# Optimization experiments

Hardware: AMD Instinct MI355X
Metric: run time of the kernel (lower is better)

Reference implementation:

```python
import jax, jax.numpy as jnp
import numpy as np
import math

B, S, D = 16, 4096, 64

def setup_inputs() -> dict:
    key = jax.random.key(0)
    kq, kk, kv = jax.random.split(key, 3)
    query = jax.random.normal(kq, (B, S, D), dtype=jnp.float32)
    k_ = jax.random.normal(kk, (B, S, D), dtype=jnp.float32)
    value = jax.random.normal(kv, (B, S, D), dtype=jnp.float32)
    # causal mask: 1 = allowed, 0 = masked (set to -inf), broadcast over batch
    mask = jnp.tril(jnp.ones((S, S), dtype=jnp.int32))[None, :, :]
    return {"query": query, "key": k_, "value": value, "mask": mask, "key_dim": D}

def reference(query, key, value, mask, key_dim):
    # scores: [B, S, S] = Q @ K^T / sqrt(dk)
    scores = jnp.einsum('bqd,bkd->bqk', query, key) / math.sqrt(key_dim)
    scores = jnp.where(mask == 0, -jnp.inf, scores)
    attn = jax.nn.softmax(scores, axis=-1)
    return jnp.einsum('bqk,bkd->bqd', attn, value)
```

## Files before the change

### kernel.cpp

```cpp
#include <hip/hip_runtime.h>

typedef _Float16 half8 __attribute__((ext_vector_type(8)));
typedef float f32x4 __attribute__((ext_vector_type(4)));
typedef unsigned int uint32x2 __attribute__((ext_vector_type(2)));

union Frag { half8 v; unsigned int u32[4]; uint4 u4; };
union Pack4 { _Float16 h[4]; unsigned int u[2]; };

constexpr int S = 4096;
constexpr int D = 64;
constexpr int NB = 16;
constexpr int LTS = 72;

__device__ __forceinline__ float ex2(float x) {
#if __has_builtin(__builtin_amdgcn_exp2f)
    return __builtin_amdgcn_exp2f(x);
#else
    return exp2f(x);
#endif
}

__global__ __launch_bounds__(256)
void prep_kernel(const float* __restrict__ K, const float* __restrict__ V,
                 _Float16* __restrict__ K16, _Float16* __restrict__ VT) {
    __shared__ float tl[64 * 66];
    const int tid = threadIdx.x;
    const int s0 = blockIdx.x * 64;
    const int b  = blockIdx.y;
    const float* Kb = K + ((size_t)b * S + s0) * D;
    const float* Vb = V + ((size_t)b * S + s0) * D;
    _Float16* K16b = K16 + ((size_t)b * S + s0) * D;

    #pragma unroll
    for (int i = 0; i < 2; ++i) {
        int e8 = tid + 256 * i;
        float4 a = ((const float4*)Kb)[2 * e8];
        float4 c = ((const float4*)Kb)[2 * e8 + 1];
        Frag f;
        f.v[0]=(_Float16)a.x; f.v[1]=(_Float16)a.y; f.v[2]=(_Float16)a.z; f.v[3]=(_Float16)a.w;
        f.v[4]=(_Float16)c.x; f.v[5]=(_Float16)c.y; f.v[6]=(_Float16)c.z; f.v[7]=(_Float16)c.w;
        ((uint4*)K16b)[e8] = f.u4;
    }
    #pragma unroll
    for (int i = 0; i < 4; ++i) {
        int fi = tid + 256 * i;
        int r = fi >> 4, c4 = (fi & 15) << 2;
        float4 v = *(const float4*)(Vb + (size_t)r * D + c4);
        float2* p = (float2*)&tl[r * 66 + c4];
        p[0] = make_float2(v.x, v.y);
        p[1] = make_float2(v.z, v.w);
    }
    __syncthreads();
    _Float16* VTb = VT + (size_t)b * D * S;
    #pragma unroll
    for (int i = 0; i < 2; ++i) {
        int fi = tid + 256 * i;
        int d = fi >> 3, s8 = (fi & 7) << 3;
        Frag f;
        #pragma unroll
        for (int j = 0; j < 8; ++j) f.v[j] = (_Float16)tl[(s8 + j) * 66 + d];
        *(uint4*)(VTb + (size_t)d * S + s0 + s8) = f.u4;
    }
}

template <int SPLIT>
__device__ __forceinline__
void fattn_body(const float* __restrict__ Q, const _Float16* __restrict__ K16,
                const _Float16* __restrict__ VT16, float* __restrict__ Out,
                _Float16* __restrict__ OP, float* __restrict__ LP,
                int b, int J, int t0, int t1, int h) {
    __shared__ __align__(16) _Float16 kt[64 * LTS];
    __shared__ __align__(16) _Float16 vt[64 * LTS];

    const int tid  = threadIdx.x;
    const int lane = tid & 63;
    const int wave = tid >> 6;
    const int ln   = lane & 15;
    const int quad = lane >> 4;

    const float* Qb = Q + (size_t)b * S * D;
    const _Float16* Kb = K16 + (size_t)b * S * D;
    const _Float16* VTb = VT16 + (size_t)b * D * S;

    const float qscale = 0.125f * 1.44269504088896340736f;
    const int qrow_base = J * 128 + wave * 32;
    const int tw = (qrow_base + 31) >> 6;

    Frag qf[2][2];
    #pragma unroll
    for (int qg = 0; qg < 2; ++qg) {
        const float* qrow = Qb + (size_t)(qrow_base + qg * 16 + ln) * D + quad * 8;
        #pragma unroll
        for (int ks = 0; ks < 2; ++ks) {
            float4 a = *(const float4*)(qrow + ks * 32);
            float4 c = *(const float4*)(qrow + ks * 32 + 4);
            Frag f;
            f.v[0]=(_Float16)(a.x*qscale); f.v[1]=(_Float16)(a.y*qscale);
            f.v[2]=(_Float16)(a.z*qscale); f.v[3]=(_Float16)(a.w*qscale);
            f.v[4]=(_Float16)(c.x*qscale); f.v[5]=(_Float16)(c.y*qscale);
            f.v[6]=(_Float16)(c.z*qscale); f.v[7]=(_Float16)(c.w*qscale);
            qf[qg][ks] = f;
        }
    }

    f32x4 o[2][4] = {};
    float l_acc[2] = {0.f, 0.f};

    for (int t = t0; t < t1; ++t) {
        const int k0 = t * 64;
        __syncthreads();

        #pragma unroll
        for (int i = 0; i < 2; ++i) {
            int fi = tid + 256 * i;
            int r = fi >> 3, c8 = (fi & 7) << 3;
            uint4 kk = *(const uint4*)(Kb + (size_t)(k0 + r) * D + c8);
            uint4 vv = *(const uint4*)(VTb + (size_t)r * S + k0 + c8);
            *(uint4*)(kt + r * LTS + c8) = kk;
            *(uint4*)(vt + r * LTS + c8) = vv;
        }
        __syncthreads();

        #pragma unroll
        for (int ks = 0; ks < 2; ++ks) {
            unsigned w[2][2][2];
            #pragma unroll
            for (int cl = 0; cl < 2; ++cl) {
                const int ct = ks * 2 + cl;
                Frag kf0, kf1;
                kf0.u4 = *(const uint4*)(kt + (ct * 16 + ln) * LTS + quad * 8);
                kf1.u4 = *(const uint4*)(kt + (ct * 16 + ln) * LTS + 32 + quad * 8);
                #pragma unroll
                for (int qg = 0; qg < 2; ++qg) {
                    f32x4 acc = {0.f, 0.f, 0.f, 0.f};
                    acc = __builtin_amdgcn_mfma_f32_16x16x32_f16(kf0.v, qf[qg][0].v, acc, 0, 0, 0);
                    acc = __builtin_amdgcn_mfma_f32_16x16x32_f16(kf1.v, qf[qg][1].v, acc, 0, 0, 0);
                    if (t >= tw) {
                        int keyb = k0 + ct * 16 + quad * 4;
                        int qrow = qrow_base + qg * 16 + ln;
                        #pragma unroll
                        for (int r = 0; r < 4; ++r)
                            if (keyb + r > qrow) acc[r] = -1e30f;
                    }
                    float p0 = ex2(acc[0]), p1 = ex2(acc[1]);
                    float p2 = ex2(acc[2]), p3 = ex2(acc[3]);
                    l_acc[qg] += (p0 + p1) + (p2 + p3);
                    Pack4 pk;
                    pk.h[0] = (_Float16)p0; pk.h[1] = (_Float16)p1;
                    pk.h[2] = (_Float16)p2; pk.h[3] = (_Float16)p3;
                    w[qg][cl][0] = pk.u[0];
                    w[qg][cl][1] = pk.u[1];
                }
            }

            Frag pf[2];
            #pragma unroll
            for (int qg = 0; qg < 2; ++qg) {
                unsigned x0 = w[qg][0][0], y0 = w[qg][1][0];
                unsigned x1 = w[qg][0][1], y1 = w[qg][1][1];
#if __has_builtin(__builtin_amdgcn_permlane32_swap) && __has_builtin(__builtin_amdgcn_permlane16_swap)
                uint32x2 r;
                r = __builtin_amdgcn_permlane32_swap(x0, y0, false, false); x0 = r[0]; y0 = r[1];
                r = __builtin_amdgcn_permlane32_swap(x1, y1, false, false); x1 = r[0]; y1 = r[1];
                r = __builtin_amdgcn_permlane16_swap(x0, y0, false, false); x0 = r[0]; y0 = r[1];
                r = __builtin_amdgcn_permlane16_swap(x1, y1, false, false); x1 = r[0]; y1 = r[1];
#else
                asm volatile("s_nop 1\n\tv_permlane32_swap_b32 %0, %1\n\ts_nop 1"
                             : "+v"(x0), "+v"(y0));
                asm volatile("v_permlane32_swap_b32 %0, %1\n\ts_nop 1"
                             : "+v"(x1), "+v"(y1));
                asm volatile("v_permlane16_swap_b32 %0, %1\n\ts_nop 1"
                             : "+v"(x0), "+v"(y0));
                asm volatile("v_permlane16_swap_b32 %0, %1\n\ts_nop 1"
                             : "+v"(x1), "+v"(y1));
#endif
                pf[qg].u32[0] = x0; pf[qg].u32[1] = x1;
                pf[qg].u32[2] = y0; pf[qg].u32[3] = y1;
            }

            #pragma unroll
            for (int sub = 0; sub < 4; ++sub) {
                Frag vf;
                vf.u4 = *(const uint4*)(vt + (sub * 16 + ln) * LTS + ks * 32 + quad * 8);
                #pragma unroll
                for (int qg = 0; qg < 2; ++qg)
                    o[qg][sub] = __builtin_amdgcn_mfma_f32_16x16x32_f16(pf[qg].v, vf.v, o[qg][sub], 0, 0, 0);
            }
        }
    }

    float lf[2];
    #pragma unroll
    for (int qg = 0; qg < 2; ++qg) {
        float x = l_acc[qg];
        x += __shfl_xor(x, 16, 64);
        x += __shfl_xor(x, 32, 64);
        lf[qg] = x;
    }

    if (SPLIT) {
        _Float16* OPb = OP + (size_t)(((b * 32 + J) * 4 + h)) * 8192;
        float* LPb = LP + (size_t)(((b * 32 + J) * 4 + h)) * 128;
        #pragma unroll
        for (int qg = 0; qg < 2; ++qg) {
            if (quad == 0) LPb[wave * 32 + qg * 16 + ln] = lf[qg];
            #pragma unroll
            for (int r = 0; r < 4; ++r) {
                float lrow = __shfl(lf[qg], quad * 4 + r, 64);
                float inv = (lrow > 0.f) ? (1.0f / lrow) : 0.f;
                #pragma unroll
                for (int sub = 0; sub < 4; ++sub)
                    OPb[(wave * 32 + qg * 16 + quad * 4 + r) * 64 + sub * 16 + ln] =
                        (_Float16)(o[qg][sub][r] * inv);
            }
        }
    } else {
        float* Ob = Out + (size_t)b * S * D;
        #pragma unroll
        for (int qg = 0; qg < 2; ++qg) {
            #pragma unroll
            for (int r = 0; r < 4; ++r) {
                float lrow = __shfl(lf[qg], quad * 4 + r, 64);
                float inv = 1.0f / lrow;
                #pragma unroll
                for (int sub = 0; sub < 4; ++sub)
                    Ob[(size_t)(qrow_base + qg * 16 + quad * 4 + r) * D + sub * 16 + ln] =
                        o[qg][sub][r] * inv;
            }
        }
    }
}

__global__ __launch_bounds__(256, 4)
void fattn_split_kernel(const float* __restrict__ Q, const _Float16* __restrict__ K16,
                        const _Float16* __restrict__ VT16,
                        _Float16* __restrict__ OP, float* __restrict__ LP) {
    const int bx = blockIdx.x;
    const int J = 31 - (bx >> 6);
    const int h = (bx >> 4) & 3;
    const int b = bx & 15;
    const int n  = 2 * J + 2;
    const int t0 = (h * n) >> 2;
    const int t1 = ((h + 1) * n) >> 2;
    fattn_body<1>(Q, K16, VT16, nullptr, OP, LP, b, J, t0, t1, h);
}

__global__ __launch_bounds__(256, 4)
void fattn_kernel(const float* __restrict__ Q, const _Float16* __restrict__ K16,
                  const _Float16* __restrict__ VT16, float* __restrict__ Out) {
    const int bx = blockIdx.x;
    const int J = 31 - (bx >> 4);
    const int b = bx & 15;
    fattn_body<0>(Q, K16, VT16, Out, nullptr, nullptr, b, J, 0, 2 * J + 2, 0);
}

__global__ __launch_bounds__(256)
void reduce_kernel(const _Float16* __restrict__ OP, const float* __restrict__ LP,
                   float* __restrict__ Out) {
    const int rb = blockIdx.x;
    const int b  = rb & 15;
    const int J  = rb >> 4;
    const int tid = threadIdx.x;
    const _Float16* p = OP + (size_t)(b * 32 + J) * 4 * 8192;
    const float* l = LP + (size_t)(b * 32 + J) * 4 * 128;
    float* Ob = Out + (size_t)b * S * D + (size_t)J * 8192;
    #pragma unroll
    for (int i = 0; i < 4; ++i) {
        int e8 = tid + 256 * i;
        int q  = e8 >> 3;
        float lw[4], lsum = 0.f;
        #pragma unroll
        for (int hh = 0; hh < 4; ++hh) { lw[hh] = l[hh * 128 + q]; lsum += lw[hh]; }
        float inv = 1.0f / lsum;
        float acc[8] = {};
        #pragma unroll
        for (int hh = 0; hh < 4; ++hh) {
            half8 v = *(const half8*)(p + (size_t)hh * 8192 + e8 * 8);
            #pragma unroll
            for (int j = 0; j < 8; ++j) acc[j] += lw[hh] * (float)v[j];
        }
        float4 r0, r1;
        r0.x = acc[0]*inv; r0.y = acc[1]*inv; r0.z = acc[2]*inv; r0.w = acc[3]*inv;
        r1.x = acc[4]*inv; r1.y = acc[5]*inv; r1.z = acc[6]*inv; r1.w = acc[7]*inv;
        ((float4*)Ob)[2 * e8]     = r0;
        ((float4*)Ob)[2 * e8 + 1] = r1;
    }
}

extern "C" void kernel_launch(void* const* d_in, const int* in_sizes, int n_in,
                              void* d_out, int out_size, void* d_ws, size_t ws_size,
                              hipStream_t stream) {
    const float* Q = (const float*)d_in[0];
    const float* K = (const float*)d_in[1];
    const float* V = (const float*)d_in[2];
    float* O = (float*)d_out;

    const size_t prepBytes = (size_t)NB * S * D * 2;
    _Float16* K16  = (_Float16*)d_ws;
    _Float16* VT16 = (_Float16*)((char*)d_ws + prepBytes);

    const size_t opOff = 2 * prepBytes;
    const size_t opBytes = (size_t)NB * 32 * 4 * 8192 * 2;
    const size_t lpOff = opOff + opBytes;
    const size_t lpBytes = (size_t)NB * 32 * 4 * 128 * 4;
    const size_t need = lpOff + lpBytes;

    hipLaunchKernelGGL(prep_kernel, dim3(S / 64, NB), dim3(256), 0, stream, K, V, K16, VT16);

    if (ws_size >= need) {
        _Float16* OP = (_Float16*)((char*)d_ws + opOff);
        float* LP = (float*)((char*)d_ws + lpOff);
        hipLaunchKernelGGL(fattn_split_kernel, dim3(128 * NB), dim3(256), 0, stream,
                           Q, K16, VT16, OP, LP);
        hipLaunchKernelGGL(reduce_kernel, dim3(32 * NB), dim3(256), 0, stream, OP, LP, O);
    } else {
        hipLaunchKernelGGL(fattn_kernel, dim3(32 * NB), dim3(256), 0, stream, Q, K16, VT16, O);
    }
}
```

Before: 187.6 us.

## Prefetch next K/V tile into registers and pack probabilities with cvt_pkrtz

Global loads of the next K and V^T tile are issued into registers right after the shared-memory barrier, so their latency overlaps the current tile's MFMA and exp work. Each iteration then only stores the already-loaded registers into LDS. Separately, the fp32-to-fp16 conversion of probabilities uses packed round-toward-zero conversion, halving the conversion instructions. The prefetch costs extra registers, which may lower occupancy, and round-toward-zero changes the rounding of P slightly.

Result: no change. 186.6 us (-0.5%).

```diff
diff --git a/kernel.cpp b/kernel.cpp
--- a/kernel.cpp
+++ b/kernel.cpp
@@ -1,11 +1,13 @@
 #include <hip/hip_runtime.h>
 
 typedef _Float16 half8 __attribute__((ext_vector_type(8)));
+typedef __fp16 fp16x2 __attribute__((ext_vector_type(2)));
 typedef float f32x4 __attribute__((ext_vector_type(4)));
 typedef unsigned int uint32x2 __attribute__((ext_vector_type(2)));
 
 union Frag { half8 v; unsigned int u32[4]; uint4 u4; };
 union Pack4 { _Float16 h[4]; unsigned int u[2]; };
+union H2U { fp16x2 h; unsigned int u; };
 
 constexpr int S = 4096;
 constexpr int D = 64;
@@ -106,20 +108,27 @@
     f32x4 o[2][4] = {};
     float l_acc[2] = {0.f, 0.f};
 
+    const int r0_ = tid >> 3,         c8_0 = (tid & 7) << 3;
+    const int r1_ = (tid + 256) >> 3, c8_1 = ((tid + 256) & 7) << 3;
+    uint4 pk0, pk1, pv0, pv1;
+    auto issue = [&](int tt) {
+        const int kk0 = tt * 64;
+        pk0 = *(const uint4*)(Kb + (size_t)(kk0 + r0_) * D + c8_0);
+        pv0 = *(const uint4*)(VTb + (size_t)r0_ * S + kk0 + c8_0);
+        pk1 = *(const uint4*)(Kb + (size_t)(kk0 + r1_) * D + c8_1);
+        pv1 = *(const uint4*)(VTb + (size_t)r1_ * S + kk0 + c8_1);
+    };
+    if (t0 < t1) issue(t0);
+
     for (int t = t0; t < t1; ++t) {
         const int k0 = t * 64;
         __syncthreads();
-
-        #pragma unroll
-        for (int i = 0; i < 2; ++i) {
-            int fi = tid + 256 * i;
-            int r = fi >> 3, c8 = (fi & 7) << 3;
-            uint4 kk = *(const uint4*)(Kb + (size_t)(k0 + r) * D + c8);
-            uint4 vv = *(const uint4*)(VTb + (size_t)r * S + k0 + c8);
-            *(uint4*)(kt + r * LTS + c8) = kk;
-            *(uint4*)(vt + r * LTS + c8) = vv;
-        }
+        *(uint4*)(kt + r0_ * LTS + c8_0) = pk0;
+        *(uint4*)(vt + r0_ * LTS + c8_0) = pv0;
+        *(uint4*)(kt + r1_ * LTS + c8_1) = pk1;
+        *(uint4*)(vt + r1_ * LTS + c8_1) = pv1;
         __syncthreads();
+        if (t + 1 < t1) issue(t + 1);
 
         #pragma unroll
         for (int ks = 0; ks < 2; ++ks) {
@@ -145,11 +154,19 @@
                     float p0 = ex2(acc[0]), p1 = ex2(acc[1]);
                     float p2 = ex2(acc[2]), p3 = ex2(acc[3]);
                     l_acc[qg] += (p0 + p1) + (p2 + p3);
+#if __has_builtin(__builtin_amdgcn_cvt_pkrtz)
+                    H2U c0, c1;
+                    c0.h = __builtin_amdgcn_cvt_pkrtz(p0, p1);
+                    c1.h = __builtin_amdgcn_cvt_pkrtz(p2, p3);
+                    w[qg][cl][0] = c0.u;
+                    w[qg][cl][1] = c1.u;
+#else
                     Pack4 pk;
                     pk.h[0] = (_Float16)p0; pk.h[1] = (_Float16)p1;
                     pk.h[2] = (_Float16)p2; pk.h[3] = (_Float16)p3;
                     w[qg][cl][0] = pk.u[0];
                     w[qg][cl][1] = pk.u[1];
+#endif
                 }
             }
 
```
